# Performance work log

Hardware: AMD Instinct MI355X
Metric: run time of the kernel (lower is better)

## Reference

```python
import jax, jax.numpy as jnp
import numpy as np

MASK_TOKEN = 0.0
TO_TAKE_PERC = 0.15
MASK_OR_SAME_PERC = 0.8


def setup_inputs() -> dict:
    key = jax.random.key(0)
    batch_patches = jax.random.normal(key, (32, 4096, 768), dtype=jnp.float32)
    return {"batch_patches": batch_patches}


def _instance_mask(key, num_patches, n_take, p):
    # Faithful to Masker.patch_indexing:
    #   idx = randperm(N)[:n]; bern ~ Bernoulli(p); idx *= bern; keep nonzero.
    # Net effect: patch i is masked iff i was sampled, its bernoulli draw is 1,
    # and i != 0 (the original's idx*bern trick can never mask index 0).
    k_perm, k_bern = jax.random.split(key)
    idx = jax.random.permutation(k_perm, num_patches)[:n_take]          # [n]
    bern = jax.random.bernoulli(k_bern, p, (n_take,))                    # [n]
    keep = bern & (idx != 0)
    return jnp.zeros((num_patches,), dtype=bool).at[idx].max(keep)       # [N]


def reference(batch_patches):
    B, N, _ = batch_patches.shape
    n_take = int(N * TO_TAKE_PERC)
    keys = jax.random.split(jax.random.key(42), B)
    # One batched RNG + scatter instead of a per-instance Python loop.
    masks = jax.vmap(lambda k: _instance_mask(k, N, n_take, MASK_OR_SAME_PERC))(keys)  # [B, N] bool
    masked = jnp.where(masks[:, :, None], jnp.asarray(MASK_TOKEN, batch_patches.dtype), batch_patches)
    # Original returns (patches, list-of-index-lists); ragged lists are not
    # jit-able, so we return the equivalent dense boolean mask instead.
    return masked, masks
```

## Files before the change

kernel.cpp:

```cpp
#include <hip/hip_runtime.h>
#include <stdint.h>


namespace {

constexpr int kB = 32;
constexpr int kN = 4096;
constexpr int kD = 768;
constexpr int kTake = 614;
constexpr size_t kMaskOff = (size_t)kB * kN * kD;

__device__ __forceinline__ uint32_t rotl32(uint32_t v, int d) {
  return (v << d) | (v >> (32 - d));
}

__device__ __forceinline__ void tf2x32(uint32_t k0, uint32_t k1,
                                       uint32_t x0, uint32_t x1,
                                       uint32_t &o0, uint32_t &o1) {
  const uint32_t k2 = k0 ^ k1 ^ 0x1BD11BDAu;
  x0 += k0; x1 += k1;
#define TF_R(r) { x0 += x1; x1 = rotl32(x1, (r)); x1 ^= x0; }
  TF_R(13) TF_R(15) TF_R(26) TF_R(6)   x0 += k1; x1 += k2 + 1u;
  TF_R(17) TF_R(29) TF_R(16) TF_R(24)  x0 += k2; x1 += k0 + 2u;
  TF_R(13) TF_R(15) TF_R(26) TF_R(6)   x0 += k0; x1 += k1 + 3u;
  TF_R(17) TF_R(29) TF_R(16) TF_R(24)  x0 += k1; x1 += k2 + 4u;
  TF_R(13) TF_R(15) TF_R(26) TF_R(6)   x0 += k2; x1 += k0 + 5u;
#undef TF_R
  o0 = x0; o1 = x1;
}

__device__ __forceinline__ uint32_t tf_bits(uint32_t k0, uint32_t k1,
                                            uint32_t i) {
  uint32_t a, b;
  tf2x32(k0, k1, 0u, i, a, b);
  return a ^ b;
}

__device__ __forceinline__ void bitonic4096(uint64_t *sk, int tid) {
  for (int k = 2; k <= 4096; k <<= 1) {
    for (int j = k >> 1; j > 0; j >>= 1) {
      __syncthreads();
      const int jm1 = j - 1;
#pragma unroll
      for (int c = tid; c < 2048; c += 1024) {
        const int i = ((c & ~jm1) << 1) | (c & jm1);
        const int p = i | j;
        const uint64_t a = sk[i];
        const uint64_t b = sk[p];
        const bool up = (i & k) == 0;
        if ((a > b) == up) { sk[i] = b; sk[p] = a; }
      }
    }
  }
  __syncthreads();
}

}

extern "C" __global__ __launch_bounds__(1024) void masker_mask_kernel(
    float *__restrict__ maskf) {
  __shared__ uint64_t sk[4096];
  __shared__ uint32_t smask[4096];
  const int b = blockIdx.x;
  const int tid = threadIdx.x;

  for (int i = tid; i < kN; i += 1024) smask[i] = 0u;

  uint32_t kb0, kb1, kp0, kp1, kr0, kr1, k10, k11, s10, s11, s20, s21;
  tf2x32(0u, 42u, 0u, (uint32_t)b, kb0, kb1);
  tf2x32(kb0, kb1, 0u, 0u, kp0, kp1);
  tf2x32(kb0, kb1, 0u, 1u, kr0, kr1);
  tf2x32(kp0, kp1, 0u, 0u, k10, k11);
  tf2x32(kp0, kp1, 0u, 1u, s10, s11);
  tf2x32(k10, k11, 0u, 1u, s20, s21);

  for (int j = tid; j < kN; j += 1024) {
    const uint32_t bits = tf_bits(s10, s11, (uint32_t)j);
    sk[j] = ((uint64_t)bits << 12) | (uint32_t)j;
  }
  bitonic4096(sk, tid);

#pragma unroll
  for (int i = 0; i < 4; ++i) {
    const int p = tid + i * 1024;
    const uint32_t x1v = (uint32_t)(sk[p] & 0xFFFu);
    const uint32_t bits = tf_bits(s20, s21, (uint32_t)p);
    sk[p] = ((uint64_t)bits << 24) | ((uint64_t)p << 12) | x1v;
  }
  bitonic4096(sk, tid);

  if (tid < kTake) {
    const uint32_t v = (uint32_t)(sk[tid] & 0xFFFu);
    const uint32_t ub = tf_bits(kr0, kr1, (uint32_t)tid);
    const float u = __uint_as_float((ub >> 9) | 0x3f800000u) - 1.0f;
    if (u < 0.8f && v != 0u) smask[v] = 1u;
  }
  __syncthreads();

  float *row = maskf + (size_t)b * kN;
  for (int n = tid; n < kN; n += 1024) row[n] = smask[n] ? 1.0f : 0.0f;
}

extern "C" __global__ __launch_bounds__(256) void masker_apply_kernel(
    const float4 *__restrict__ in, float4 *__restrict__ out,
    const float *__restrict__ maskf) {
  const int gid = blockIdx.x * 256 + threadIdx.x;
  const int row = gid / (kD / 4);
  const float m = maskf[row];
  float4 v = in[gid];
  if (m != 0.0f) { v.x = 0.f; v.y = 0.f; v.z = 0.f; v.w = 0.f; }
  out[gid] = v;
}

extern "C" void kernel_launch(void* const* d_in, const int* in_sizes, int n_in,
                              void* d_out, int out_size, void* d_ws,
                              size_t ws_size, hipStream_t stream) {
  (void)in_sizes; (void)n_in; (void)out_size; (void)d_ws; (void)ws_size;
  const float* in = (const float*)d_in[0];
  float* out = (float*)d_out;
  float* maskf = out + kMaskOff;

  masker_mask_kernel<<<kB, 1024, 0, stream>>>(maskf);

  const int n4 = (kB * kN * kD) / 4;
  masker_apply_kernel<<<n4 / 256, 256, 0, stream>>>(
      (const float4*)in, (float4*)out, maskf);
}
```

Baseline: 678.4 us.

## Replace bitonic sorts with bucketed counting-rank sort and skip masked-row loads

The two 4096-element bitonic sorts in the mask kernel are replaced by a bucket scatter on the top 10 bits of the random key, followed by rank computation within each bucket. This avoids the many barrier-separated bitonic passes. The apply kernel now reads input only for unmasked rows, so masked rows skip their global load. The mask kernel runs on only 32 blocks and the apply kernel is bandwidth bound, so the sort change mainly shortens the small prologue, and the skipped loads save roughly the masked fraction of read traffic.

```diff
diff --git a/kernel.cpp b/kernel.cpp
--- a/kernel.cpp
+++ b/kernel.cpp
@@ -9,6 +9,7 @@
 constexpr int kD = 768;
 constexpr int kTake = 614;
 constexpr size_t kMaskOff = (size_t)kB * kN * kD;
+constexpr int kBkt = 1024;
 
 __device__ __forceinline__ uint32_t rotl32(uint32_t v, int d) {
   return (v << d) | (v >> (32 - d));
@@ -36,35 +37,22 @@
   return a ^ b;
 }
 
-__device__ __forceinline__ void bitonic4096(uint64_t *sk, int tid) {
-  for (int k = 2; k <= 4096; k <<= 1) {
-    for (int j = k >> 1; j > 0; j >>= 1) {
-      __syncthreads();
-      const int jm1 = j - 1;
-#pragma unroll
-      for (int c = tid; c < 2048; c += 1024) {
-        const int i = ((c & ~jm1) << 1) | (c & jm1);
-        const int p = i | j;
-        const uint64_t a = sk[i];
-        const uint64_t b = sk[p];
-        const bool up = (i & k) == 0;
-        if ((a > b) == up) { sk[i] = b; sk[p] = a; }
-      }
-    }
-  }
-  __syncthreads();
-}
-
 }
 
 extern "C" __global__ __launch_bounds__(1024) void masker_mask_kernel(
     float *__restrict__ maskf) {
-  __shared__ uint64_t sk[4096];
-  __shared__ uint32_t smask[4096];
+  __shared__ uint64_t karr[kN];
+  __shared__ uint32_t scnt[kBkt];
+  __shared__ uint32_t scur[kBkt];
+  __shared__ uint32_t sbase[kBkt + 1];
+  __shared__ uint16_t sx1[kN];
+  __shared__ uint32_t swsum[16];
+  __shared__ unsigned long long smaskbits[kN / 64];
+
   const int b = blockIdx.x;
   const int tid = threadIdx.x;
-
-  for (int i = tid; i < kN; i += 1024) smask[i] = 0u;
+  const int lane = tid & 63;
+  const int wid = tid >> 6;
 
   uint32_t kb0, kb1, kp0, kp1, kr0, kr1, k10, k11, s10, s11, s20, s21;
   tf2x32(0u, 42u, 0u, (uint32_t)b, kb0, kb1);
@@ -74,31 +62,115 @@
   tf2x32(kp0, kp1, 0u, 1u, s10, s11);
   tf2x32(k10, k11, 0u, 1u, s20, s21);
 
-  for (int j = tid; j < kN; j += 1024) {
+  auto scan_bases = [&]() {
+    uint32_t x = scnt[tid];
+#pragma unroll
+    for (int d = 1; d < 64; d <<= 1) {
+      uint32_t y = __shfl_up(x, d, 64);
+      if (lane >= d) x += y;
+    }
+    if (lane == 63) swsum[wid] = x;
+    __syncthreads();
+    if (wid == 0) {
+      uint32_t w = (lane < 16) ? swsum[lane] : 0u;
+#pragma unroll
+      for (int d = 1; d < 16; d <<= 1) {
+        uint32_t y = __shfl_up(w, d, 64);
+        if (lane >= d) w += y;
+      }
+      if (lane < 16) swsum[lane] = w;
+    }
+    __syncthreads();
+    const uint32_t off = (wid > 0) ? swsum[wid - 1] : 0u;
+    sbase[tid + 1] = x + off;
+    if (tid == 0) sbase[0] = 0u;
+    __syncthreads();
+  };
+
+  scnt[tid] = 0u;
+  scur[tid] = 0u;
+  __syncthreads();
+
+  uint32_t mybits[4];
+#pragma unroll
+  for (int e = 0; e < 4; ++e) {
+    const int j = tid + e * 1024;
     const uint32_t bits = tf_bits(s10, s11, (uint32_t)j);
-    sk[j] = ((uint64_t)bits << 12) | (uint32_t)j;
-  }
-  bitonic4096(sk, tid);
-
-#pragma unroll
-  for (int i = 0; i < 4; ++i) {
-    const int p = tid + i * 1024;
-    const uint32_t x1v = (uint32_t)(sk[p] & 0xFFFu);
+    mybits[e] = bits;
+    atomicAdd(&scnt[bits >> 22], 1u);
+  }
+  __syncthreads();
+  scan_bases();
+
+#pragma unroll
+  for (int e = 0; e < 4; ++e) {
+    const int j = tid + e * 1024;
+    const uint32_t bits = mybits[e];
+    const uint32_t slot = sbase[bits >> 22] + atomicAdd(&scur[bits >> 22], 1u);
+    karr[slot] = ((uint64_t)bits << 12) | (uint32_t)j;
+  }
+  __syncthreads();
+
+#pragma unroll
+  for (int e = 0; e < 4; ++e) {
+    const int j = tid + e * 1024;
+    const uint64_t myk = ((uint64_t)mybits[e] << 12) | (uint32_t)j;
+    const uint32_t bkt = mybits[e] >> 22;
+    uint32_t r = sbase[bkt];
+    const uint32_t end = sbase[bkt + 1];
+    for (uint32_t t = sbase[bkt]; t < end; ++t) r += (karr[t] < myk) ? 1u : 0u;
+    sx1[r] = (uint16_t)j;
+  }
+  __syncthreads();
+
+  scnt[tid] = 0u;
+  scur[tid] = 0u;
+  if (tid < kN / 64) smaskbits[tid] = 0ull;
+  __syncthreads();
+
+#pragma unroll
+  for (int e = 0; e < 4; ++e) {
+    const int p = tid + e * 1024;
     const uint32_t bits = tf_bits(s20, s21, (uint32_t)p);
-    sk[p] = ((uint64_t)bits << 24) | ((uint64_t)p << 12) | x1v;
-  }
-  bitonic4096(sk, tid);
-
-  if (tid < kTake) {
-    const uint32_t v = (uint32_t)(sk[tid] & 0xFFFu);
-    const uint32_t ub = tf_bits(kr0, kr1, (uint32_t)tid);
-    const float u = __uint_as_float((ub >> 9) | 0x3f800000u) - 1.0f;
-    if (u < 0.8f && v != 0u) smask[v] = 1u;
+    mybits[e] = bits;
+    atomicAdd(&scnt[bits >> 22], 1u);
+  }
+  __syncthreads();
+  scan_bases();
+
+#pragma unroll
+  for (int e = 0; e < 4; ++e) {
+    const int p = tid + e * 1024;
+    const uint32_t bits = mybits[e];
+    const uint32_t slot = sbase[bits >> 22] + atomicAdd(&scur[bits >> 22], 1u);
+    karr[slot] = ((uint64_t)bits << 12) | (uint32_t)p;
+  }
+  __syncthreads();
+
+#pragma unroll
+  for (int e = 0; e < 4; ++e) {
+    const int p = tid + e * 1024;
+    const uint64_t myk = ((uint64_t)mybits[e] << 12) | (uint32_t)p;
+    const uint32_t bkt = mybits[e] >> 22;
+    uint32_t r = sbase[bkt];
+    const uint32_t end = sbase[bkt + 1];
+    for (uint32_t t = sbase[bkt]; t < end; ++t) r += (karr[t] < myk) ? 1u : 0u;
+    if (r < (uint32_t)kTake) {
+      const uint32_t v = sx1[p];
+      const uint32_t ub = tf_bits(kr0, kr1, r);
+      const float u = __uint_as_float((ub >> 9) | 0x3f800000u) - 1.0f;
+      if (u < 0.8f && v != 0u)
+        atomicOr(&smaskbits[v >> 6], 1ull << (v & 63));
+    }
   }
   __syncthreads();
 
   float *row = maskf + (size_t)b * kN;
-  for (int n = tid; n < kN; n += 1024) row[n] = smask[n] ? 1.0f : 0.0f;
+#pragma unroll
+  for (int e = 0; e < 4; ++e) {
+    const int n = tid + e * 1024;
+    row[n] = ((smaskbits[n >> 6] >> (n & 63)) & 1ull) ? 1.0f : 0.0f;
+  }
 }
 
 extern "C" __global__ __launch_bounds__(256) void masker_apply_kernel(
@@ -107,8 +179,8 @@
   const int gid = blockIdx.x * 256 + threadIdx.x;
   const int row = gid / (kD / 4);
   const float m = maskf[row];
-  float4 v = in[gid];
-  if (m != 0.0f) { v.x = 0.f; v.y = 0.f; v.z = 0.f; v.w = 0.f; }
+  float4 v = make_float4(0.f, 0.f, 0.f, 0.f);
+  if (m == 0.0f) v = in[gid];
   out[gid] = v;
 }
 
```

Result: faster. 628.1 us (-7.4%).
